# Performance work log

Hardware: AMD Instinct MI355X
Metric: run time of the kernel (lower is better)

## Reference

```python
import jax, jax.numpy as jnp
import numpy as np

G = 256        # num_networks
IN_F = 256
OUT_F = 256
N = 262144     # total rows, sum(counts) == N
PAD = 2048     # static per-network padding (>= max count)


def setup_inputs() -> dict:
    key = jax.random.key(0)
    kw, kb, kx = jax.random.split(key, 3)
    scale = 1.0 / np.sqrt(IN_F)
    weight = jax.random.normal(kw, (G, OUT_F, IN_F), jnp.float32) * scale
    bias = jax.random.normal(kb, (G, 1, OUT_F), jnp.float32) * scale
    x = jax.random.normal(kx, (N, IN_F), jnp.float32)
    # irregular per-network row counts summing exactly to N, all < PAD
    rng = np.random.default_rng(0)
    counts = rng.multinomial(N, np.ones(G) / G).astype(np.int32)
    assert counts.max() < PAD and counts.sum() == N
    return {"weight": weight, "bias": bias, "x": x, "counts": jnp.asarray(counts)}


def reference(weight, bias, x, counts):
    # Rows of x are contiguous segments: network g owns rows [offs[g], offs[g]+counts[g]).
    n = x.shape[0]
    offs = jnp.concatenate([jnp.zeros((1,), counts.dtype), jnp.cumsum(counts)])  # [G+1]
    row = jnp.arange(n)
    net_id = jnp.searchsorted(offs[1:], row, side="right")        # [N] network of each row
    rank = row - offs[net_id]                                      # position within segment
    # scatter rows into padded per-network buffer [G, PAD, IN_F]
    buf = jnp.zeros((G, PAD, x.shape[1]), x.dtype).at[net_id, rank].set(x)
    # grouped batched GEMM: y = x_g @ W_g^T + b_g
    y = jnp.einsum("gpi,goi->gpo", buf, weight) + bias             # [G, PAD, OUT_F]
    return y[net_id, rank]                                         # [N, OUT_F]
```

## Files before the change

kernel.cpp:

```cpp
#include <hip/hip_runtime.h>
#include <stdint.h>

#define NG 256
#define KF 256
#define OF 256
#define BM 128
#define BK 32
#define NKT 8
#define NTILES 16
#define NTH 512

using f32x4  = __attribute__((ext_vector_type(4))) float;
using bf16x8 = __attribute__((ext_vector_type(8))) __bf16;
using u16x8  = __attribute__((ext_vector_type(8))) unsigned short;

__device__ __forceinline__ unsigned short f2bf(float f) {
  unsigned u = __builtin_bit_cast(unsigned, f);
  u += 0x7fffu + ((u >> 16) & 1u);
  return (unsigned short)(u >> 16);
}

__global__ void scan_kernel(const int* __restrict__ counts, int* __restrict__ offs) {
  __shared__ int s[NG];
  int t = threadIdx.x;
  s[t] = counts[t];
  __syncthreads();
  #pragma unroll
  for (int d = 1; d < NG; d <<= 1) {
    int u = (t >= d) ? s[t - d] : 0;
    __syncthreads();
    s[t] += u;
    __syncthreads();
  }
  if (t == 0) offs[0] = 0;
  offs[t + 1] = s[t];
}

__global__ __launch_bounds__(512)
void wconv_kernel(const float* __restrict__ w, unsigned short* __restrict__ img) {
  int tid = blockIdx.x * 512 + threadIdx.x;
  int s  = tid & 3;
  int o  = (tid >> 2) & 255;
  int kt = (tid >> 10) & 7;
  int g  = tid >> 13;
  int k0 = kt * 32 + ((s ^ (o & 3)) << 3);
  const float* src = w + ((size_t)(g * 256 + o) * 256 + k0);
  f32x4 a = *(const f32x4*)src;
  f32x4 b = *(const f32x4*)(src + 4);
  u16x8 r;
  r[0]=f2bf(a[0]); r[1]=f2bf(a[1]); r[2]=f2bf(a[2]); r[3]=f2bf(a[3]);
  r[4]=f2bf(b[0]); r[5]=f2bf(b[1]); r[6]=f2bf(b[2]); r[7]=f2bf(b[3]);
  *(u16x8*)(img + (size_t)tid * 8) = r;
}

template<bool PRECONV>
__global__ __launch_bounds__(NTH, 4)
void gemm_kernel(const float* __restrict__ x,
                 const float* __restrict__ wf32,
                 const unsigned short* __restrict__ wimg,
                 const float* __restrict__ bias,
                 const int* __restrict__ offs,
                 float* __restrict__ out)
{
  __shared__ __align__(16) unsigned short Bs[3][OF * BK];

  const int g      = blockIdx.y;
  const int r0     = offs[g];
  const int cnt    = offs[g + 1] - r0;
  const int tstart = blockIdx.x * BM;
  if (tstart >= cnt) return;
  const int mrows = min(BM, cnt - tstart);
  const int row0  = r0 + tstart;

  const int tid  = threadIdx.x;
  const int lane = tid & 63;
  const int w    = tid >> 6;
  const int lrow = lane & 15;
  const int lk   = lane >> 4;

  const int arow = w * 16 + lrow;
  const int ar   = row0 + min(arow, mrows - 1);
  const float* aptr = x + (size_t)ar * KF + lk * 8;

  f32x4 areg[2][2];
  auto issueA = [&](int kt) {
    const float* p = aptr + kt * BK;
    areg[kt & 1][0] = *(const f32x4*)(p);
    areg[kt & 1][1] = *(const f32x4*)(p + 4);
  };
  auto mkfrag = [&](int kt) -> bf16x8 {
    f32x4 lo = areg[kt & 1][0], hi = areg[kt & 1][1];
    u16x8 r;
    r[0]=f2bf(lo[0]); r[1]=f2bf(lo[1]); r[2]=f2bf(lo[2]); r[3]=f2bf(lo[3]);
    r[4]=f2bf(hi[0]); r[5]=f2bf(hi[1]); r[6]=f2bf(hi[2]); r[7]=f2bf(hi[3]);
    return __builtin_bit_cast(bf16x8, r);
  };

  auto issueB = [&](int kt, int buf) {
    const char* sb = (const char*)wimg + ((size_t)g << 17) + (size_t)kt * 16384;
    #pragma unroll
    for (int r = 0; r < 2; ++r) {
      int c = w * 2 + r;
      __builtin_amdgcn_global_load_lds(
          (const __attribute__((address_space(1))) void*)(sb + c * 1024 + lane * 16),
          (__attribute__((address_space(3))) void*)((char*)&Bs[buf][0] + c * 1024),
          16, 0, 0);
    }
  };

  f32x4 acc[16] = {};
  const int slot  = lk ^ (lrow & 3);
  const int bbase = lrow * 32 + slot * 8;

  auto compute = [&](int kt, int buf) {
    bf16x8 af = mkfrag(kt);
    #pragma unroll
    for (int n = 0; n < 16; ++n) {
      bf16x8 wf = *(const bf16x8*)&Bs[buf][n * 512 + bbase];
      acc[n] = __builtin_amdgcn_mfma_f32_16x16x32_bf16(wf, af, acc[n], 0, 0, 0);
    }
  };

  if (PRECONV) {
    issueA(0);
    issueB(0, 0);
    issueB(1, 1);
    #pragma unroll
    for (int kt = 0; kt < NKT; ++kt) {
      if (kt < NKT - 1) asm volatile("s_waitcnt vmcnt(2)" ::: "memory");
      else              asm volatile("s_waitcnt vmcnt(0)" ::: "memory");
      __builtin_amdgcn_s_barrier();
      __builtin_amdgcn_sched_barrier(0);
      if (kt + 1 < NKT) issueA(kt + 1);
      if (kt + 2 < NKT) issueB(kt + 2, (kt + 2) % 3);
      __builtin_amdgcn_sched_barrier(0);
      compute(kt, kt % 3);
    }
  } else {
    #pragma unroll
    for (int kt = 0; kt < NKT; ++kt) {
      u16x8 v[2];
      #pragma unroll
      for (int r = 0; r < 2; ++r) {
        int sl = tid + r * 512;
        int o  = sl >> 2, s = sl & 3;
        int k  = kt * 32 + ((s ^ (o & 3)) << 3);
        const float* src = wf32 + ((size_t)(g * 256 + o) * 256 + k);
        f32x4 a = *(const f32x4*)src;
        f32x4 b = *(const f32x4*)(src + 4);
        v[r][0]=f2bf(a[0]); v[r][1]=f2bf(a[1]); v[r][2]=f2bf(a[2]); v[r][3]=f2bf(a[3]);
        v[r][4]=f2bf(b[0]); v[r][5]=f2bf(b[1]); v[r][6]=f2bf(b[2]); v[r][7]=f2bf(b[3]);
      }
      __syncthreads();
      #pragma unroll
      for (int r = 0; r < 2; ++r) {
        int sl = tid + r * 512;
        *(u16x8*)&Bs[0][sl * 8] = v[r];
      }
      __syncthreads();
      issueA(kt);
      compute(kt, 0);
    }
  }

  if (arow < mrows) {
    float* orow = out + (size_t)(row0 + arow) * OF;
    const float* brow = bias + g * OF;
    #pragma unroll
    for (int n = 0; n < 16; ++n) {
      f32x4 b4 = *(const f32x4*)&brow[n * 16 + lk * 4];
      f32x4 v  = acc[n] + b4;
      *(f32x4*)&orow[n * 16 + lk * 4] = v;
    }
  }
}

extern "C" void kernel_launch(void* const* d_in, const int* in_sizes, int n_in,
                              void* d_out, int out_size, void* d_ws, size_t ws_size,
                              hipStream_t stream) {
  const float* weight = (const float*)d_in[0];
  const float* bias   = (const float*)d_in[1];
  const float* x      = (const float*)d_in[2];
  const int*   counts = (const int*)d_in[3];
  float* out = (float*)d_out;

  int* offs = (int*)d_ws;
  unsigned short* wimg = (unsigned short*)((char*)d_ws + 4096);
  const size_t need = 4096 + (size_t)NG * 8 * 16384;

  scan_kernel<<<1, 256, 0, stream>>>(counts, offs);

  if (ws_size >= need) {
    wconv_kernel<<<(NG * 8 * 256 * 4) / 512, 512, 0, stream>>>(weight, wimg);
    gemm_kernel<true><<<dim3(NTILES, NG), NTH, 0, stream>>>(x, weight, wimg, bias, offs, out);
  } else {
    gemm_kernel<false><<<dim3(NTILES, NG), NTH, 0, stream>>>(x, weight, wimg, bias, offs, out);
  }
}
```

Baseline: 240.5 us.

## Retile GEMM waves into 2x4 grid of 64x64 tiles with new LDS swizzle

The wave work split changes from eight waves each owning 16 rows across all 256 output columns to a 2x4 wave grid where each wave owns a 64x64 tile. This cuts LDS reads of the weight fragments per MFMA by a factor of four. In exchange, each x row is loaded and converted to bf16 by four waves instead of one. The weight swizzle is changed to (o>>1)&3 to adjust LDS bank mapping, the bias is folded into the accumulator initialization, and the vmcnt waits are retuned for the larger A prefetch.

```diff
diff --git a/kernel.cpp b/kernel.cpp
--- a/kernel.cpp
+++ b/kernel.cpp
@@ -39,11 +39,12 @@
 __global__ __launch_bounds__(512)
 void wconv_kernel(const float* __restrict__ w, unsigned short* __restrict__ img) {
   int tid = blockIdx.x * 512 + threadIdx.x;
-  int s  = tid & 3;
+  int sp = tid & 3;
   int o  = (tid >> 2) & 255;
   int kt = (tid >> 10) & 7;
   int g  = tid >> 13;
-  int k0 = kt * 32 + ((s ^ (o & 3)) << 3);
+  int s  = sp ^ ((o >> 1) & 3);
+  int k0 = kt * 32 + s * 8;
   const float* src = w + ((size_t)(g * 256 + o) * 256 + k0);
   f32x4 a = *(const f32x4*)src;
   f32x4 b = *(const f32x4*)(src + 4);
@@ -74,67 +75,87 @@
 
   const int tid  = threadIdx.x;
   const int lane = tid & 63;
-  const int w    = tid >> 6;
+  const int wid  = tid >> 6;
+  const int wm   = wid >> 2;
+  const int wn   = wid & 3;
   const int lrow = lane & 15;
   const int lk   = lane >> 4;
-
-  const int arow = w * 16 + lrow;
-  const int ar   = row0 + min(arow, mrows - 1);
-  const float* aptr = x + (size_t)ar * KF + lk * 8;
-
-  f32x4 areg[2][2];
+  const int slot = lk ^ ((lrow >> 1) & 3);
+
+  const float* abase = x + (size_t)row0 * KF;
+  int aoff[4];
+  #pragma unroll
+  for (int m = 0; m < 4; ++m) {
+    int r = min(wm * 64 + m * 16 + lrow, mrows - 1);
+    aoff[m] = r * KF + lk * 8;
+  }
+
+  f32x4 areg[4][2];
   auto issueA = [&](int kt) {
-    const float* p = aptr + kt * BK;
-    areg[kt & 1][0] = *(const f32x4*)(p);
-    areg[kt & 1][1] = *(const f32x4*)(p + 4);
-  };
-  auto mkfrag = [&](int kt) -> bf16x8 {
-    f32x4 lo = areg[kt & 1][0], hi = areg[kt & 1][1];
+    #pragma unroll
+    for (int m = 0; m < 4; ++m) {
+      const float* p = abase + aoff[m] + kt * BK;
+      areg[m][0] = *(const f32x4*)(p);
+      areg[m][1] = *(const f32x4*)(p + 4);
+    }
+  };
+
+  auto issueB = [&](int kt, int buf) {
+    const unsigned short* sb = wimg + (((size_t)(g * 8 + kt)) << 13);
+    #pragma unroll
+    for (int r = 0; r < 2; ++r) {
+      int c = wid * 2 + r;
+      __builtin_amdgcn_global_load_lds(
+          (const __attribute__((address_space(1))) void*)(sb + c * 512 + lane * 8),
+          (__attribute__((address_space(3))) void*)((char*)&Bs[buf][0] + c * 1024),
+          16, 0, 0);
+    }
+  };
+
+  f32x4 acc[4][4];
+  #pragma unroll
+  for (int n = 0; n < 4; ++n) {
+    f32x4 b4 = *(const f32x4*)&bias[g * OF + wn * 64 + n * 16 + lk * 4];
+    #pragma unroll
+    for (int m = 0; m < 4; ++m) acc[n][m] = b4;
+  }
+
+  auto cvtA = [&](int m) -> bf16x8 {
+    f32x4 lo = areg[m][0], hi = areg[m][1];
     u16x8 r;
     r[0]=f2bf(lo[0]); r[1]=f2bf(lo[1]); r[2]=f2bf(lo[2]); r[3]=f2bf(lo[3]);
     r[4]=f2bf(hi[0]); r[5]=f2bf(hi[1]); r[6]=f2bf(hi[2]); r[7]=f2bf(hi[3]);
     return __builtin_bit_cast(bf16x8, r);
   };
 
-  auto issueB = [&](int kt, int buf) {
-    const char* sb = (const char*)wimg + ((size_t)g << 17) + (size_t)kt * 16384;
-    #pragma unroll
-    for (int r = 0; r < 2; ++r) {
-      int c = w * 2 + r;
-      __builtin_amdgcn_global_load_lds(
-          (const __attribute__((address_space(1))) void*)(sb + c * 1024 + lane * 16),
-          (__attribute__((address_space(3))) void*)((char*)&Bs[buf][0] + c * 1024),
-          16, 0, 0);
-    }
-  };
-
-  f32x4 acc[16] = {};
-  const int slot  = lk ^ (lrow & 3);
-  const int bbase = lrow * 32 + slot * 8;
-
-  auto compute = [&](int kt, int buf) {
-    bf16x8 af = mkfrag(kt);
-    #pragma unroll
-    for (int n = 0; n < 16; ++n) {
-      bf16x8 wf = *(const bf16x8*)&Bs[buf][n * 512 + bbase];
-      acc[n] = __builtin_amdgcn_mfma_f32_16x16x32_bf16(wf, af, acc[n], 0, 0, 0);
+  auto compute = [&](const bf16x8* xf, int buf) {
+    #pragma unroll
+    for (int n = 0; n < 4; ++n) {
+      int o16 = (wn * 64 + n * 16 + lrow) * 32 + slot * 8;
+      bf16x8 wf = *(const bf16x8*)&Bs[buf][o16];
+      #pragma unroll
+      for (int m = 0; m < 4; ++m)
+        acc[n][m] = __builtin_amdgcn_mfma_f32_16x16x32_bf16(wf, xf[m], acc[n][m], 0, 0, 0);
     }
   };
 
   if (PRECONV) {
+    issueB(0, 0);
     issueA(0);
-    issueB(0, 0);
     issueB(1, 1);
     #pragma unroll
     for (int kt = 0; kt < NKT; ++kt) {
-      if (kt < NKT - 1) asm volatile("s_waitcnt vmcnt(2)" ::: "memory");
-      else              asm volatile("s_waitcnt vmcnt(0)" ::: "memory");
+      if (kt + 1 < NKT) asm volatile("s_waitcnt vmcnt(10)" ::: "memory");
+      else              asm volatile("s_waitcnt vmcnt(8)"  ::: "memory");
       __builtin_amdgcn_s_barrier();
       __builtin_amdgcn_sched_barrier(0);
+      if (kt + 2 < NKT) issueB(kt + 2, (kt + 2) % 3);
+      bf16x8 xf[4];
+      #pragma unroll
+      for (int m = 0; m < 4; ++m) xf[m] = cvtA(m);
       if (kt + 1 < NKT) issueA(kt + 1);
-      if (kt + 2 < NKT) issueB(kt + 2, (kt + 2) % 3);
       __builtin_amdgcn_sched_barrier(0);
-      compute(kt, kt % 3);
+      compute(xf, kt % 3);
     }
   } else {
     #pragma unroll
@@ -142,10 +163,10 @@
       u16x8 v[2];
       #pragma unroll
       for (int r = 0; r < 2; ++r) {
-        int sl = tid + r * 512;
-        int o  = sl >> 2, s = sl & 3;
-        int k  = kt * 32 + ((s ^ (o & 3)) << 3);
-        const float* src = wf32 + ((size_t)(g * 256 + o) * 256 + k);
+        int sl = tid * 2 + r;
+        int o = sl >> 2, sp = sl & 3;
+        int s = sp ^ ((o >> 1) & 3);
+        const float* src = wf32 + ((size_t)(g * 256 + o) * 256 + kt * 32 + s * 8);
         f32x4 a = *(const f32x4*)src;
         f32x4 b = *(const f32x4*)(src + 4);
         v[r][0]=f2bf(a[0]); v[r][1]=f2bf(a[1]); v[r][2]=f2bf(a[2]); v[r][3]=f2bf(a[3]);
@@ -153,24 +174,25 @@
       }
       __syncthreads();
       #pragma unroll
-      for (int r = 0; r < 2; ++r) {
-        int sl = tid + r * 512;
-        *(u16x8*)&Bs[0][sl * 8] = v[r];
-      }
+      for (int r = 0; r < 2; ++r)
+        *(u16x8*)&Bs[0][(tid * 2 + r) * 8] = v[r];
       __syncthreads();
       issueA(kt);
-      compute(kt, 0);
-    }
-  }
-
-  if (arow < mrows) {
-    float* orow = out + (size_t)(row0 + arow) * OF;
-    const float* brow = bias + g * OF;
-    #pragma unroll
-    for (int n = 0; n < 16; ++n) {
-      f32x4 b4 = *(const f32x4*)&brow[n * 16 + lk * 4];
-      f32x4 v  = acc[n] + b4;
-      *(f32x4*)&orow[n * 16 + lk * 4] = v;
+      bf16x8 xf[4];
+      #pragma unroll
+      for (int m = 0; m < 4; ++m) xf[m] = cvtA(m);
+      compute(xf, 0);
+    }
+  }
+
+  #pragma unroll
+  for (int m = 0; m < 4; ++m) {
+    int r = wm * 64 + m * 16 + lrow;
+    if (r < mrows) {
+      float* orow = out + (size_t)(row0 + r) * OF + wn * 64 + lk * 4;
+      #pragma unroll
+      for (int n = 0; n < 4; ++n)
+        *(f32x4*)&orow[n * 16] = acc[n][m];
     }
   }
 }
```

Measured after the change: 725.6 us. 3.02x slower.

## Load full per-network weight into LDS once and process 256 rows per block

Applied to the files above, without the earlier changes.

Each block now loads the whole 256x256 bf16 weight of its network (128 KB) into LDS in one shot, instead of streaming K-slices through a triple buffer. Each block covers 256 rows in two 128-row sub-passes, so every weight load is reused twice as much and there are half as many blocks. The bias is folded into the accumulator init, and the LDS swizzle changes to a (row>>1)-based XOR to avoid bank conflicts. The cost is lower occupancy (launch bounds 2, 128 KB LDS per block), no overlap of weight loading with compute, and fewer blocks for the final partial tiles.

```diff
diff --git a/kernel.cpp b/kernel.cpp
--- a/kernel.cpp
+++ b/kernel.cpp
@@ -4,10 +4,8 @@
 #define NG 256
 #define KF 256
 #define OF 256
-#define BM 128
-#define BK 32
-#define NKT 8
-#define NTILES 16
+#define PAD 2048
+#define RPB 256
 #define NTH 512
 
 using f32x4  = __attribute__((ext_vector_type(4))) float;
@@ -39,11 +37,12 @@
 __global__ __launch_bounds__(512)
 void wconv_kernel(const float* __restrict__ w, unsigned short* __restrict__ img) {
   int tid = blockIdx.x * 512 + threadIdx.x;
-  int s  = tid & 3;
+  int sp = tid & 3;
   int o  = (tid >> 2) & 255;
   int kt = (tid >> 10) & 7;
   int g  = tid >> 13;
-  int k0 = kt * 32 + ((s ^ (o & 3)) << 3);
+  int s  = sp ^ ((o >> 1) & 3);
+  int k0 = kt * 32 + s * 8;
   const float* src = w + ((size_t)(g * 256 + o) * 256 + k0);
   f32x4 a = *(const f32x4*)src;
   f32x4 b = *(const f32x4*)(src + 4);
@@ -54,7 +53,7 @@
 }
 
 template<bool PRECONV>
-__global__ __launch_bounds__(NTH, 4)
+__global__ __launch_bounds__(NTH, 2)
 void gemm_kernel(const float* __restrict__ x,
                  const float* __restrict__ wf32,
                  const unsigned short* __restrict__ wimg,
@@ -62,14 +61,14 @@
                  const int* __restrict__ offs,
                  float* __restrict__ out)
 {
-  __shared__ __align__(16) unsigned short Bs[3][OF * BK];
+  __shared__ __align__(16) unsigned short Ws[8 * 8192];
 
   const int g      = blockIdx.y;
   const int r0     = offs[g];
   const int cnt    = offs[g + 1] - r0;
-  const int tstart = blockIdx.x * BM;
+  const int tstart = blockIdx.x * RPB;
   if (tstart >= cnt) return;
-  const int mrows = min(BM, cnt - tstart);
+  const int mrows = min(RPB, cnt - tstart);
   const int row0  = r0 + tstart;
 
   const int tid  = threadIdx.x;
@@ -77,100 +76,99 @@
   const int w    = tid >> 6;
   const int lrow = lane & 15;
   const int lk   = lane >> 4;
-
-  const int arow = w * 16 + lrow;
-  const int ar   = row0 + min(arow, mrows - 1);
-  const float* aptr = x + (size_t)ar * KF + lk * 8;
-
-  f32x4 areg[2][2];
-  auto issueA = [&](int kt) {
-    const float* p = aptr + kt * BK;
-    areg[kt & 1][0] = *(const f32x4*)(p);
-    areg[kt & 1][1] = *(const f32x4*)(p + 4);
-  };
-  auto mkfrag = [&](int kt) -> bf16x8 {
-    f32x4 lo = areg[kt & 1][0], hi = areg[kt & 1][1];
-    u16x8 r;
-    r[0]=f2bf(lo[0]); r[1]=f2bf(lo[1]); r[2]=f2bf(lo[2]); r[3]=f2bf(lo[3]);
-    r[4]=f2bf(hi[0]); r[5]=f2bf(hi[1]); r[6]=f2bf(hi[2]); r[7]=f2bf(hi[3]);
-    return __builtin_bit_cast(bf16x8, r);
-  };
-
-  auto issueB = [&](int kt, int buf) {
-    const char* sb = (const char*)wimg + ((size_t)g << 17) + (size_t)kt * 16384;
-    #pragma unroll
-    for (int r = 0; r < 2; ++r) {
-      int c = w * 2 + r;
-      __builtin_amdgcn_global_load_lds(
-          (const __attribute__((address_space(1))) void*)(sb + c * 1024 + lane * 16),
-          (__attribute__((address_space(3))) void*)((char*)&Bs[buf][0] + c * 1024),
-          16, 0, 0);
-    }
-  };
-
-  f32x4 acc[16] = {};
-  const int slot  = lk ^ (lrow & 3);
-  const int bbase = lrow * 32 + slot * 8;
-
-  auto compute = [&](int kt, int buf) {
-    bf16x8 af = mkfrag(kt);
-    #pragma unroll
-    for (int n = 0; n < 16; ++n) {
-      bf16x8 wf = *(const bf16x8*)&Bs[buf][n * 512 + bbase];
-      acc[n] = __builtin_amdgcn_mfma_f32_16x16x32_bf16(wf, af, acc[n], 0, 0, 0);
-    }
-  };
+  const int slot = lk ^ ((lrow >> 1) & 3);
 
   if (PRECONV) {
-    issueA(0);
-    issueB(0, 0);
-    issueB(1, 1);
+    const char* src = (const char*)wimg + ((size_t)g << 17);
     #pragma unroll
-    for (int kt = 0; kt < NKT; ++kt) {
-      if (kt < NKT - 1) asm volatile("s_waitcnt vmcnt(2)" ::: "memory");
-      else              asm volatile("s_waitcnt vmcnt(0)" ::: "memory");
-      __builtin_amdgcn_s_barrier();
-      __builtin_amdgcn_sched_barrier(0);
-      if (kt + 1 < NKT) issueA(kt + 1);
-      if (kt + 2 < NKT) issueB(kt + 2, (kt + 2) % 3);
-      __builtin_amdgcn_sched_barrier(0);
-      compute(kt, kt % 3);
+    for (int i = 0; i < 16; ++i) {
+      int base = i * 8192 + w * 1024;
+      __builtin_amdgcn_global_load_lds(
+          (const __attribute__((address_space(1))) void*)(src + base + lane * 16),
+          (__attribute__((address_space(3))) void*)((char*)Ws + base),
+          16, 0, 0);
     }
   } else {
     #pragma unroll
-    for (int kt = 0; kt < NKT; ++kt) {
-      u16x8 v[2];
-      #pragma unroll
-      for (int r = 0; r < 2; ++r) {
-        int sl = tid + r * 512;
-        int o  = sl >> 2, s = sl & 3;
-        int k  = kt * 32 + ((s ^ (o & 3)) << 3);
-        const float* src = wf32 + ((size_t)(g * 256 + o) * 256 + k);
-        f32x4 a = *(const f32x4*)src;
-        f32x4 b = *(const f32x4*)(src + 4);
-        v[r][0]=f2bf(a[0]); v[r][1]=f2bf(a[1]); v[r][2]=f2bf(a[2]); v[r][3]=f2bf(a[3]);
-        v[r][4]=f2bf(b[0]); v[r][5]=f2bf(b[1]); v[r][6]=f2bf(b[2]); v[r][7]=f2bf(b[3]);
-      }
-      __syncthreads();
-      #pragma unroll
-      for (int r = 0; r < 2; ++r) {
-        int sl = tid + r * 512;
-        *(u16x8*)&Bs[0][sl * 8] = v[r];
-      }
-      __syncthreads();
-      issueA(kt);
-      compute(kt, 0);
+    for (int i = 0; i < 16; ++i) {
+      int sl = i * 512 + tid;
+      int kt = sl >> 10, o = (sl >> 2) & 255, sp = sl & 3;
+      int s  = sp ^ ((o >> 1) & 3);
+      const float* p = wf32 + (size_t)(g * 256 + o) * 256 + kt * 32 + s * 8;
+      f32x4 a = *(const f32x4*)p;
+      f32x4 b = *(const f32x4*)(p + 4);
+      u16x8 r;
+      r[0]=f2bf(a[0]); r[1]=f2bf(a[1]); r[2]=f2bf(a[2]); r[3]=f2bf(a[3]);
+      r[4]=f2bf(b[0]); r[5]=f2bf(b[1]); r[6]=f2bf(b[2]); r[7]=f2bf(b[3]);
+      *(u16x8*)((char*)Ws + (size_t)sl * 16) = r;
     }
   }
 
-  if (arow < mrows) {
-    float* orow = out + (size_t)(row0 + arow) * OF;
-    const float* brow = bias + g * OF;
+  __builtin_amdgcn_sched_barrier(0);
+  const int arow0 = min(w * 16 + lrow, mrows - 1);
+  const float* ap0 = x + (size_t)(row0 + arow0) * KF + lk * 8;
+  f32x4 af[16];
+  #pragma unroll
+  for (int kt = 0; kt < 8; ++kt) {
+    af[kt * 2]     = *(const f32x4*)(ap0 + kt * 32);
+    af[kt * 2 + 1] = *(const f32x4*)(ap0 + kt * 32 + 4);
+  }
+  __builtin_amdgcn_sched_barrier(0);
+
+  if (PRECONV) {
+    asm volatile("s_waitcnt vmcnt(16)" ::: "memory");
+    __builtin_amdgcn_s_barrier();
+    __builtin_amdgcn_sched_barrier(0);
+  } else {
+    __syncthreads();
+  }
+
+  const float* bp = bias + g * OF + lk * 4;
+
+  #pragma unroll
+  for (int sub = 0; sub < 2; ++sub) {
+    const int rowbase = sub * 128 + w * 16;
+    if (rowbase >= mrows) continue;
+
+    if (sub == 1) {
+      const int arow = min(rowbase + lrow, mrows - 1);
+      const float* ap = x + (size_t)(row0 + arow) * KF + lk * 8;
+      #pragma unroll
+      for (int kt = 0; kt < 8; ++kt) {
+        af[kt * 2]     = *(const f32x4*)(ap + kt * 32);
+        af[kt * 2 + 1] = *(const f32x4*)(ap + kt * 32 + 4);
+      }
+    }
+
+    bf16x8 xf[8];
     #pragma unroll
-    for (int n = 0; n < 16; ++n) {
-      f32x4 b4 = *(const f32x4*)&brow[n * 16 + lk * 4];
-      f32x4 v  = acc[n] + b4;
-      *(f32x4*)&orow[n * 16 + lk * 4] = v;
+    for (int kt = 0; kt < 8; ++kt) {
+      f32x4 lo = af[kt * 2], hi = af[kt * 2 + 1];
+      u16x8 r;
+      r[0]=f2bf(lo[0]); r[1]=f2bf(lo[1]); r[2]=f2bf(lo[2]); r[3]=f2bf(lo[3]);
+      r[4]=f2bf(hi[0]); r[5]=f2bf(hi[1]); r[6]=f2bf(hi[2]); r[7]=f2bf(hi[3]);
+      xf[kt] = __builtin_bit_cast(bf16x8, r);
+    }
+
+    f32x4 acc[16];
+    #pragma unroll
+    for (int n = 0; n < 16; ++n) acc[n] = *(const f32x4*)(bp + n * 16);
+
+    #pragma unroll
+    for (int kt = 0; kt < 8; ++kt) {
+      #pragma unroll
+      for (int n = 0; n < 16; ++n) {
+        bf16x8 wf = *(const bf16x8*)&Ws[kt * 8192 + ((n * 16 + lrow) * 4 + slot) * 8];
+        acc[n] = __builtin_amdgcn_mfma_f32_16x16x32_bf16(wf, xf[kt], acc[n], 0, 0, 0);
+      }
+    }
+
+    const int r = rowbase + lrow;
+    if (r < mrows) {
+      float* orow = out + (size_t)(row0 + r) * OF + lk * 4;
+      #pragma unroll
+      for (int n = 0; n < 16; ++n)
+        *(f32x4*)&orow[n * 16] = acc[n];
     }
   }
 }
@@ -192,8 +190,8 @@
 
   if (ws_size >= need) {
     wconv_kernel<<<(NG * 8 * 256 * 4) / 512, 512, 0, stream>>>(weight, wimg);
-    gemm_kernel<true><<<dim3(NTILES, NG), NTH, 0, stream>>>(x, weight, wimg, bias, offs, out);
+    gemm_kernel<true><<<dim3(PAD / RPB, NG), NTH, 0, stream>>>(x, weight, wimg, bias, offs, out);
   } else {
-    gemm_kernel<false><<<dim3(NTILES, NG), NTH, 0, stream>>>(x, weight, wimg, bias, offs, out);
+    gemm_kernel<false><<<dim3(PAD / RPB, NG), NTH, 0, stream>>>(x, weight, wimg, bias, offs, out);
   }
 }
```

Result: slower. 277.2 us (+15.3%).
